# Kernel tuning notes

Hardware: AMD Instinct MI355X
Metric: run time of the kernel (lower is better)

The kernel has to match this reference:

```python
import jax, jax.numpy as jnp
import numpy as np
from jax import lax

B, S, E, DF, H, L, V, T = 32, 512, 512, 2048, 8, 2, 30000, 12
START, STOP = 10, 11
NEG = -10000.0


def setup_inputs() -> dict:
    key = jax.random.key(0)
    ks = jax.random.split(key, 12)
    g = lambda i, shape, sc=0.02: jax.random.normal(ks[i], shape, jnp.float32) * sc
    trans = jax.random.normal(ks[9], (T, T), jnp.float32)
    trans = trans.at[START, :].set(NEG).at[:, STOP].set(NEG)
    return {
        "sentence": jax.random.randint(ks[0], (B, S), 0, V),
        "seq_len": jax.random.randint(ks[1], (B,), 1, S + 1),
        "tags": jax.random.randint(ks[2], (B, S), 0, 10),
        "emb": g(3, (V, E), 1.0),
        "attn_in_w": g(4, (L, 3 * E, E)), "attn_in_b": jnp.zeros((L, 3 * E)),
        "attn_out_w": g(5, (L, E, E)), "attn_out_b": jnp.zeros((L, E)),
        "ln1_g": jnp.ones((L, E)), "ln1_b": jnp.zeros((L, E)),
        "ln2_g": jnp.ones((L, E)), "ln2_b": jnp.zeros((L, E)),
        "ff1_w": g(6, (L, DF, E)), "ff1_b": jnp.zeros((L, DF)),
        "ff2_w": g(7, (L, E, DF)), "ff2_b": jnp.zeros((L, E)),
        "tag_w": g(8, (T, E)), "tag_b": jnp.zeros((T,)),
        "transitions": trans,
    }


def _ln(x, g, b):
    m = x.mean(-1, keepdims=True)
    v = ((x - m) ** 2).mean(-1, keepdims=True)
    return (x - m) / jnp.sqrt(v + 1e-5) * g + b


def _mha(x, w_in, b_in, w_out, b_out):
    b_, s_, e_ = x.shape
    d = e_ // H
    qkv = x @ w_in.T + b_in
    q, k, v = jnp.split(qkv, 3, axis=-1)
    split = lambda t: t.reshape(b_, s_, H, d).transpose(0, 2, 1, 3)
    q, k, v = split(q), split(k), split(v)
    att = jax.nn.softmax(jnp.einsum('bhqd,bhkd->bhqk', q, k) / np.sqrt(d).astype(np.float32), axis=-1)
    o = jnp.einsum('bhqk,bhkd->bhqd', att, v).transpose(0, 2, 1, 3).reshape(b_, s_, e_)
    return o @ w_out.T + b_out


def _forward_impl(sentence, seq_len, tags, emb, attn_in_w, attn_in_b, attn_out_w,
                  attn_out_b, ln1_g, ln1_b, ln2_g, ln2_b, ff1_w, ff1_b, ff2_w,
                  ff2_b, tag_w, tag_b, transitions):
    # Transformer encoder features (dropout in eval mode -> identity)
    x = emb[sentence]  # (B,S,E)
    for l in range(L):
        x = _ln(x + _mha(x, attn_in_w[l], attn_in_b[l], attn_out_w[l], attn_out_b[l]), ln1_g[l], ln1_b[l])
        h = jax.nn.relu(x @ ff1_w[l].T + ff1_b[l]) @ ff2_w[l].T + ff2_b[l]
        x = _ln(x + h, ln2_g[l], ln2_b[l])
    feats = x @ tag_w.T + tag_b  # (B,S,T)

    # CRF forward algorithm (log-semiring scan, masked by seq_len)
    alpha0 = jnp.full((B, T), NEG, feats.dtype).at[:, START].set(0.0)

    def step(alpha, xs):
        emit_t, t = xs  # emit_t: (B,T)
        new = emit_t + jax.nn.logsumexp(alpha[:, None, :] + transitions[None, :, :], axis=-1)
        return jnp.where((t < seq_len)[:, None], new, alpha), None

    alpha, _ = lax.scan(step, alpha0, (feats.transpose(1, 0, 2), jnp.arange(S)))
    fwd_score = jax.nn.logsumexp(alpha + transitions[STOP][None, :], axis=-1)  # (B,)

    # gold score (vectorized _score_sentence)
    tags_ext = jnp.concatenate([jnp.full((B, 1), START, tags.dtype), tags], axis=1)  # (B,S+1)
    mask = jnp.arange(S)[None, :] < seq_len[:, None]  # (B,S)
    trans_sc = jnp.where(mask, transitions[tags_ext[:, 1:], tags_ext[:, :-1]], 0.0).sum(-1)
    emit_sc = jnp.where(mask, jnp.take_along_axis(feats, tags[:, :, None], axis=2)[..., 0], 0.0).sum(-1)
    last_tag = jnp.take_along_axis(tags_ext, seq_len[:, None], axis=1)[:, 0]
    gold = trans_sc + emit_sc + transitions[STOP, last_tag]

    return jnp.mean(fwd_score - gold)


def reference(sentence, seq_len, tags, emb, attn_in_w, attn_in_b, attn_out_w,
              attn_out_b, ln1_g, ln1_b, ln2_g, ln2_b, ff1_w, ff1_b, ff2_w,
              ff2_b, tag_w, tag_b, transitions):
    return _forward_impl(sentence, seq_len, tags, emb, attn_in_w, attn_in_b,
                         attn_out_w, attn_out_b, ln1_g, ln1_b, ln2_g, ln2_b,
                         ff1_w, ff1_b, ff2_w, ff2_b, tag_w, tag_b, transitions)
```

## Files before the change

kernel.cpp:

```cpp
#include <hip/hip_runtime.h>
#include <hip/hip_bf16.h>

#define BB 32
#define SSZ 512
#define EE 512
#define DFF 2048
#define HH 8
#define LL 2
#define TT 12
#define START_TAG 10
#define STOP_TAG 11
#define CB 8
#define CM (CB * SSZ)
#define NCHUNK (BB / CB)
#define NBH (CB * HH)
#define NBH_ALL (BB * HH)
#define NCHK 8

typedef __hip_bfloat16 bf16;
typedef __attribute__((ext_vector_type(8))) short short8;
typedef __attribute__((ext_vector_type(4))) float f32x4;

__device__ __forceinline__ float b2f(bf16 x) { return __bfloat162float(x); }
__device__ __forceinline__ float ldw(const void* p, size_t i, bool isbf) {
  return isbf ? __bfloat162float(((const bf16*)p)[i]) : ((const float*)p)[i];
}

__device__ __forceinline__ void gl_lds16(const bf16* g, bf16* l) {
  __builtin_amdgcn_global_load_lds(
      (const __attribute__((address_space(1))) void*)g,
      (__attribute__((address_space(3))) void*)l, 16, 0, 0);
}

__device__ __forceinline__ int swz(int row, int col) {
  return row * 128 + (col ^ (((row >> 2) & 7) * 16));
}

__global__ void k_detect(const void* trans, int* dflag) {
  if (threadIdx.x == 0) {
    const unsigned short* u = (const unsigned short*)trans;
    dflag[0] = (u[START_TAG * TT] == 0xC61C && u[START_TAG * TT + 1] == 0xC61C) ? 1 : 0;
  }
}

__global__ void k_cvt(const void* src, bf16* dst, long n, const int* dflag) {
  bool isbf = dflag[0] != 0;
  for (long i = (long)blockIdx.x * 256 + threadIdx.x; i < n; i += (long)gridDim.x * 256)
    dst[i] = __float2bfloat16(ldw(src, i, isbf));
}

__global__ void k_embed(const int* sent, const void* emb, bf16* xb, const int* dflag) {
  bool isbf = dflag[0] != 0;
  int tok = blockIdx.x;
  int v = sent[tok];
  bf16* xo = xb + (size_t)tok * EE;
  for (int i = threadIdx.x; i < EE; i += 256)
    xo[i] = __float2bfloat16(ldw(emb, (size_t)v * EE + i, isbf));
}

__global__ __launch_bounds__(256) void k_mgemm(
    const bf16* __restrict__ A, const bf16* __restrict__ W,
    const void* __restrict__ bias, size_t boff, bf16* __restrict__ Cb,
    bf16* __restrict__ vtout, int M, int N, int K, int relu, const int* dflag) {
  bool isbf = dflag[0] != 0;
  __shared__ __align__(16) bf16 Sh[2 * 128 * 64];
  bf16* As = Sh;
  bf16* Bs = Sh + 128 * 64;
  const int tid = threadIdx.x;
  const int lane = tid & 63;
  const int wave = tid >> 6;
  const int wm = wave >> 1, wn = wave & 1;
  const int m0 = blockIdx.x * 128, n0 = blockIdx.y * 128;
  const int lrow = lane & 15, lk = lane >> 4;
  const int rl = lane >> 3, sl = lane & 7;

  f32x4 acc[4][4];
#pragma unroll
  for (int i = 0; i < 4; ++i)
#pragma unroll
    for (int j = 0; j < 4; ++j) acc[i][j] = (f32x4){0.f, 0.f, 0.f, 0.f};

  for (int kt = 0; kt < K; kt += 64) {
#pragma unroll
    for (int i = 0; i < 4; ++i) {
      int r = wave * 32 + i * 8 + rl;
      int gs = sl ^ (r & 7);
      gl_lds16(A + (size_t)(m0 + r) * K + kt + gs * 8, As + wave * 2048 + i * 512);
      gl_lds16(W + (size_t)(n0 + r) * K + kt + gs * 8, Bs + wave * 2048 + i * 512);
    }
    __syncthreads();
#pragma unroll
    for (int kb = 0; kb < 64; kb += 32) {
      short8 af[4], bfr[4];
#pragma unroll
      for (int mf = 0; mf < 4; ++mf) {
        int r = wm * 64 + mf * 16 + lrow;
        int ps = ((kb >> 3) + lk) ^ (r & 7);
        af[mf] = *(const short8*)&As[r * 64 + ps * 8];
      }
#pragma unroll
      for (int nf = 0; nf < 4; ++nf) {
        int r = wn * 64 + nf * 16 + lrow;
        int ps = ((kb >> 3) + lk) ^ (r & 7);
        bfr[nf] = *(const short8*)&Bs[r * 64 + ps * 8];
      }
#pragma unroll
      for (int mf = 0; mf < 4; ++mf)
#pragma unroll
        for (int nf = 0; nf < 4; ++nf)
          acc[mf][nf] = __builtin_amdgcn_mfma_f32_16x16x32_bf16(
              af[mf], bfr[nf], acc[mf][nf], 0, 0, 0);
    }
    __syncthreads();
  }

  const bool vpath = (vtout != nullptr) && (n0 >= 1024);
  if (!vpath) {
#pragma unroll
    for (int nf = 0; nf < 4; ++nf) {
      int nl = wn * 64 + nf * 16 + lrow;
      float bia = ldw(bias, boff + n0 + nl, isbf);
#pragma unroll
      for (int mf = 0; mf < 4; ++mf) {
#pragma unroll
        for (int r = 0; r < 4; ++r) {
          int ml = wm * 64 + mf * 16 + lk * 4 + r;
          float v = acc[mf][nf][r] + bia;
          if (relu) v = fmaxf(v, 0.f);
          Sh[swz(ml, nl)] = __float2bfloat16(v);
        }
      }
    }
    __syncthreads();
#pragma unroll
    for (int p = 0; p < 8; ++p) {
      int row = p * 16 + (tid >> 4);
      int off = (tid & 15) * 8;
      *(uint4*)(Cb + (size_t)(m0 + row) * N + n0 + off) =
          *(const uint4*)&Sh[swz(row, off)];
    }
  } else {
#pragma unroll
    for (int nf = 0; nf < 4; ++nf) {
      int nl = wn * 64 + nf * 16 + lrow;
      float bia = ldw(bias, boff + n0 + nl, isbf);
#pragma unroll
      for (int mf = 0; mf < 4; ++mf) {
        int mlb = wm * 64 + mf * 16 + lk * 4;
        bf16 t4[4];
#pragma unroll
        for (int r = 0; r < 4; ++r) t4[r] = __float2bfloat16(acc[mf][nf][r] + bia);
        *(uint2*)&Sh[swz(nl, mlb)] = *(const uint2*)t4;
      }
    }
    __syncthreads();
    int h0 = (n0 - 1024) >> 6;
    int blb = (m0 >> 9) * 8;
    int pos0 = m0 & 511;
#pragma unroll
    for (int p = 0; p < 8; ++p) {
      int drow = p * 16 + (tid >> 4);
      int poff = (tid & 15) * 8;
      bf16* dst = vtout + ((size_t)(blb + h0 + (drow >> 6)) * 64 + (drow & 63)) * 512 +
                  pos0 + poff;
      *(uint4*)dst = *(const uint4*)&Sh[swz(drow, poff)];
    }
  }
}

#define LDK 68
#define LDP 72
__global__ __launch_bounds__(256) void k_flash(const bf16* __restrict__ qkv,
                                               const bf16* __restrict__ vt,
                                               bf16* __restrict__ ctx) {
  const int bh = blockIdx.x;
  const int bl = bh >> 3, h = bh & 7;
  const int m0 = blockIdx.y * 128;
  const int tid = threadIdx.x;
  const int lane = tid & 63;
  const int w = tid >> 6;
  const int lrow = lane & 15, lk = lane >> 4;

  __shared__ bf16 Ks[64 * LDK];
  __shared__ bf16 Vs[64 * LDK];
  __shared__ bf16 Ps[4][32 * LDP];

  short8 qf[2][2];
  {
    const bf16* Qb = qkv + (size_t)(bl * SSZ + m0 + w * 32) * 1536 + h * 64;
#pragma unroll
    for (int mf = 0; mf < 2; ++mf)
#pragma unroll
      for (int kb = 0; kb < 2; ++kb)
        qf[mf][kb] = *(const short8*)(Qb + (size_t)(mf * 16 + lrow) * 1536 + kb * 32 + lk * 8);
  }

  f32x4 acc_o[2][4];
  float lsum[2][4];
#pragma unroll
  for (int mf = 0; mf < 2; ++mf) {
#pragma unroll
    for (int nf = 0; nf < 4; ++nf) acc_o[mf][nf] = (f32x4){0.f, 0.f, 0.f, 0.f};
#pragma unroll
    for (int r = 0; r < 4; ++r) lsum[mf][r] = 0.f;
  }

  for (int kt = 0; kt < 8; ++kt) {
#pragma unroll
    for (int i = 0; i < 2; ++i) {
      int cc = tid + i * 256;
      int row = cc >> 3, seg = cc & 7;
      *(uint4*)&Ks[row * LDK + seg * 8] = *(const uint4*)(
          qkv + (size_t)(bl * SSZ + kt * 64 + row) * 1536 + 512 + h * 64 + seg * 8);
      *(uint4*)&Vs[row * LDK + seg * 8] = *(const uint4*)(
          vt + ((size_t)bh * 64 + row) * SSZ + kt * 64 + seg * 8);
    }
    __syncthreads();
    f32x4 s[2][4];
#pragma unroll
    for (int mf = 0; mf < 2; ++mf)
#pragma unroll
      for (int nf = 0; nf < 4; ++nf) s[mf][nf] = (f32x4){0.f, 0.f, 0.f, 0.f};
#pragma unroll
    for (int kb = 0; kb < 2; ++kb) {
      short8 bk[4];
#pragma unroll
      for (int nf = 0; nf < 4; ++nf)
        bk[nf] = *(const short8*)&Ks[(nf * 16 + lrow) * LDK + kb * 32 + lk * 8];
#pragma unroll
      for (int mf = 0; mf < 2; ++mf)
#pragma unroll
        for (int nf = 0; nf < 4; ++nf)
          s[mf][nf] = __builtin_amdgcn_mfma_f32_16x16x32_bf16(qf[mf][kb], bk[nf],
                                                              s[mf][nf], 0, 0, 0);
    }
#pragma unroll
    for (int mf = 0; mf < 2; ++mf)
#pragma unroll
      for (int r = 0; r < 4; ++r) {
        float p0 = __expf(0.125f * s[mf][0][r]);
        float p1 = __expf(0.125f * s[mf][1][r]);
        float p2 = __expf(0.125f * s[mf][2][r]);
        float p3 = __expf(0.125f * s[mf][3][r]);
        s[mf][0][r] = p0; s[mf][1][r] = p1; s[mf][2][r] = p2; s[mf][3][r] = p3;
        lsum[mf][r] += (p0 + p1) + (p2 + p3);
      }
#pragma unroll
    for (int mf = 0; mf < 2; ++mf)
#pragma unroll
      for (int nf = 0; nf < 4; ++nf)
#pragma unroll
        for (int r = 0; r < 4; ++r)
          Ps[w][(mf * 16 + lk * 4 + r) * LDP + nf * 16 + lrow] =
              __float2bfloat16(s[mf][nf][r]);
#pragma unroll
    for (int kb = 0; kb < 2; ++kb) {
      short8 ap[2], bv[4];
#pragma unroll
      for (int mf = 0; mf < 2; ++mf)
        ap[mf] = *(const short8*)&Ps[w][(mf * 16 + lrow) * LDP + kb * 32 + lk * 8];
#pragma unroll
      for (int nf = 0; nf < 4; ++nf)
        bv[nf] = *(const short8*)&Vs[(nf * 16 + lrow) * LDK + kb * 32 + lk * 8];
#pragma unroll
      for (int mf = 0; mf < 2; ++mf)
#pragma unroll
        for (int nf = 0; nf < 4; ++nf)
          acc_o[mf][nf] = __builtin_amdgcn_mfma_f32_16x16x32_bf16(ap[mf], bv[nf],
                                                                  acc_o[mf][nf], 0, 0, 0);
    }
    __syncthreads();
  }
#pragma unroll
  for (int mf = 0; mf < 2; ++mf) {
#pragma unroll
    for (int r = 0; r < 4; ++r) {
      float ls = lsum[mf][r];
      ls += __shfl_xor(ls, 1, 64);
      ls += __shfl_xor(ls, 2, 64);
      ls += __shfl_xor(ls, 4, 64);
      ls += __shfl_xor(ls, 8, 64);
      float inv = 1.f / ls;
      int q = m0 + w * 32 + mf * 16 + lk * 4 + r;
#pragma unroll
      for (int nf = 0; nf < 4; ++nf)
        ctx[((size_t)(bl * SSZ + q)) * EE + h * 64 + nf * 16 + lrow] =
            __float2bfloat16(acc_o[mf][nf][r] * inv);
    }
  }
}

__global__ void k_ln_res(bf16* xb, const bf16* hb, const void* g,
                         const void* be, size_t goff, const int* dflag) {
  bool isbf = dflag[0] != 0;
  int tok = blockIdx.x, tid = threadIdx.x;
  size_t base = (size_t)tok * EE;
  float v0 = b2f(xb[base + tid]) + b2f(hb[base + tid]);
  float v1 = b2f(xb[base + tid + 256]) + b2f(hb[base + tid + 256]);
  float s = v0 + v1, ss = v0 * v0 + v1 * v1;
#pragma unroll
  for (int off = 32; off > 0; off >>= 1) {
    s += __shfl_down(s, off, 64);
    ss += __shfl_down(ss, off, 64);
  }
  __shared__ float ps[4], pss[4];
  __shared__ float mean_s, rstd_s;
  int w = tid >> 6;
  if ((tid & 63) == 0) { ps[w] = s; pss[w] = ss; }
  __syncthreads();
  if (tid == 0) {
    float S_ = ps[0] + ps[1] + ps[2] + ps[3];
    float SS_ = pss[0] + pss[1] + pss[2] + pss[3];
    float mu = S_ / (float)EE;
    float var = SS_ / (float)EE - mu * mu;
    mean_s = mu;
    rstd_s = rsqrtf(var + 1e-5f);
  }
  __syncthreads();
  float mu = mean_s, rs = rstd_s;
  float r0 = (v0 - mu) * rs * ldw(g, goff + tid, isbf) + ldw(be, goff + tid, isbf);
  float r1 = (v1 - mu) * rs * ldw(g, goff + tid + 256, isbf) + ldw(be, goff + tid + 256, isbf);
  xb[base + tid] = __float2bfloat16(r0);
  xb[base + tid + 256] = __float2bfloat16(r1);
}

__global__ void k_feats(const bf16* xb, const bf16* tgw, const void* tgb,
                        float* feats, const int* dflag) {
  bool isbf = dflag[0] != 0;
  int m = blockIdx.x * 4 + (threadIdx.x >> 6);
  int lane = threadIdx.x & 63;
  uint4 raw = *(const uint4*)(xb + (size_t)m * EE + lane * 8);
  const bf16* rb = (const bf16*)&raw;
  float xv[8];
#pragma unroll
  for (int j = 0; j < 8; ++j) xv[j] = b2f(rb[j]);
#pragma unroll
  for (int t = 0; t < TT; ++t) {
    uint4 wraw = *(const uint4*)(tgw + t * EE + lane * 8);
    const bf16* wb = (const bf16*)&wraw;
    float s = 0.f;
#pragma unroll
    for (int j = 0; j < 8; ++j) s += xv[j] * b2f(wb[j]);
#pragma unroll
    for (int off = 32; off > 0; off >>= 1) s += __shfl_down(s, off, 64);
    if (lane == 0) feats[(size_t)m * TT + t] = s + ldw(tgb, t, isbf);
  }
}

__global__ void k_crf1(const float* feats, const int* seq_len, const void* trans_in,
                       float* cmat, const int* dflag) {
  bool isbf = dflag[0] != 0;
  int c = blockIdx.x, b = blockIdx.y;
  int tid = threadIdx.x;
  __shared__ float tr[144];
  __shared__ float abuf[2][144];
  if (tid < 144) tr[tid] = ldw(trans_in, tid, isbf);
  bool act = tid < 144;
  int i = tid / 12, j = tid % 12;
  if (act) abuf[0][tid] = (i == j) ? 0.f : -1e30f;
  __syncthreads();
  float trrow[12];
  if (act) {
#pragma unroll
    for (int k = 0; k < 12; ++k) trrow[k] = tr[i * 12 + k];
  }
  int len = seq_len[b];
  int t0 = c * 64;
  int t1 = min(len, t0 + 64);
  int cur = 0;
  for (int t = t0; t < t1; ++t) {
    float nv = 0.f;
    if (act) {
      float m = -1e30f, v[12];
#pragma unroll
      for (int k = 0; k < 12; ++k) {
        v[k] = trrow[k] + abuf[cur][k * 12 + j];
        m = fmaxf(m, v[k]);
      }
      float s = 0.f;
#pragma unroll
      for (int k = 0; k < 12; ++k) s += __expf(v[k] - m);
      nv = feats[((size_t)b * SSZ + t) * TT + i] + m + __logf(s);
    }
    if (act) abuf[cur ^ 1][tid] = nv;
    __syncthreads();
    cur ^= 1;
  }
  if (act) cmat[((size_t)b * NCHK + c) * 144 + tid] = abuf[cur][tid];
}

__global__ void k_crf2(const float* cmat, const float* feats, const int* tags,
                       const int* seq_len, const void* trans_in, float* bscore,
                       const int* dflag) {
  bool isbf = dflag[0] != 0;
  int b = blockIdx.x;
  int tid = threadIdx.x;
  __shared__ float tr[144];
  __shared__ float tbuf[2][144];
  __shared__ float alpha_sh[12];
  if (tid < 144) tr[tid] = ldw(trans_in, tid, isbf);
  bool act = tid < 144;
  int i = tid / 12, j = tid % 12;
  if (act) tbuf[0][tid] = cmat[((size_t)b * NCHK) * 144 + tid];
  __syncthreads();
  int cur = 0;
  for (int c = 1; c < NCHK; ++c) {
    float nv = 0.f;
    if (act) {
      const float* Cc = cmat + ((size_t)b * NCHK + c) * 144;
      float m = -1e30f, v[12];
#pragma unroll
      for (int k = 0; k < 12; ++k) {
        v[k] = Cc[i * 12 + k] + tbuf[cur][k * 12 + j];
        m = fmaxf(m, v[k]);
      }
      float s = 0.f;
#pragma unroll
      for (int k = 0; k < 12; ++k) s += __expf(v[k] - m);
      nv = m + __logf(s);
    }
    if (act) tbuf[cur ^ 1][tid] = nv;
    __syncthreads();
    cur ^= 1;
  }
  if (tid < 12) {
    float m = -1e30f, v[12];
#pragma unroll
    for (int k = 0; k < 12; ++k) {
      float a0 = (k == START_TAG) ? 0.f : -10000.f;
      v[k] = tbuf[cur][tid * 12 + k] + a0;
      m = fmaxf(m, v[k]);
    }
    float s = 0.f;
#pragma unroll
    for (int k = 0; k < 12; ++k) s += __expf(v[k] - m);
    alpha_sh[tid] = m + __logf(s);
  }
  __syncthreads();
  if (tid < 64) {
    int lane = tid;
    int len = seq_len[b];
    float part = 0.f;
    for (int s = lane; s < len; s += 64) {
      int ct = tags[b * SSZ + s];
      int pv = (s == 0) ? START_TAG : tags[b * SSZ + s - 1];
      part += tr[ct * 12 + pv] + feats[((size_t)b * SSZ + s) * TT + ct];
    }
#pragma unroll
    for (int off = 32; off > 0; off >>= 1) part += __shfl_down(part, off, 64);
    if (lane == 0) {
      float m = -1e30f;
#pragma unroll
      for (int k = 0; k < 12; ++k) m = fmaxf(m, alpha_sh[k] + tr[STOP_TAG * 12 + k]);
      float s = 0.f;
#pragma unroll
      for (int k = 0; k < 12; ++k) s += __expf(alpha_sh[k] + tr[STOP_TAG * 12 + k] - m);
      float fwd = m + __logf(s);
      int last = tags[b * SSZ + len - 1];
      bscore[b] = fwd - (part + tr[STOP_TAG * 12 + last]);
    }
  }
}

__global__ void k_final(const float* bscore, float* out) {
  int tid = threadIdx.x;
  float v = (tid < BB) ? bscore[tid] : 0.f;
#pragma unroll
  for (int off = 32; off > 0; off >>= 1) v += __shfl_down(v, off, 64);
  if (tid == 0) out[0] = v / (float)BB;
}

extern "C" void kernel_launch(void* const* d_in, const int* in_sizes, int n_in,
                              void* d_out, int out_size, void* d_ws, size_t ws_size,
                              hipStream_t stream) {
  const int* sentence = (const int*)d_in[0];
  const int* seq_len = (const int*)d_in[1];
  const int* tags = (const int*)d_in[2];
  const void* emb = d_in[3];
  const void* attn_in_w = d_in[4];
  const void* attn_in_b = d_in[5];
  const void* attn_out_w = d_in[6];
  const void* attn_out_b = d_in[7];
  const void* ln1_g = d_in[8];
  const void* ln1_b = d_in[9];
  const void* ln2_g = d_in[10];
  const void* ln2_b = d_in[11];
  const void* ff1_w = d_in[12];
  const void* ff1_b = d_in[13];
  const void* ff2_w = d_in[14];
  const void* ff2_b = d_in[15];
  const void* tag_w = d_in[16];
  const void* tag_b = d_in[17];
  const void* transitions = d_in[18];

  const int M = BB * SSZ;
  const size_t WEL = (size_t)LL * 3 * EE * EE + (size_t)LL * EE * EE +
                     (size_t)LL * DFF * EE + (size_t)LL * EE * DFF + (size_t)TT * EE;

  size_t o = 0;
  size_t f_feats = o; o += (size_t)M * TT;
  size_t f_bsc = o; o += 64;
  size_t f_cmat = o; o += (size_t)BB * NCHK * 144;
  size_t f_dflag = o; o += 16;
  size_t f_xb = o; o += (size_t)M * EE / 2;
  size_t f_hb = o; o += (size_t)M * EE / 2;
  size_t f_ctxb = o; o += (size_t)M * EE / 2;
  size_t f_act = o; o += (size_t)M * DFF / 2;
  size_t f_vt = o; o += (size_t)NBH_ALL * 64 * SSZ / 2;
  size_t f_w = o; o += (WEL + 1) / 2 + 8;
  size_t need_full = o * 4;
  bool full = ws_size >= need_full;

  float* ws = (float*)d_ws;
  if (full) {
    float* feats = ws + f_feats;
    float* bsc = ws + f_bsc;
    float* cmat = ws + f_cmat;
    int* dflag = (int*)(ws + f_dflag);
    bf16* xb = (bf16*)(ws + f_xb);
    bf16* hb = (bf16*)(ws + f_hb);
    bf16* ctxb = (bf16*)(ws + f_ctxb);
    bf16* act = (bf16*)(ws + f_act);
    bf16* vt = (bf16*)(ws + f_vt);
    bf16* w_aiw = (bf16*)(ws + f_w);
    bf16* w_aow = w_aiw + (size_t)LL * 3 * EE * EE;
    bf16* w_f1 = w_aow + (size_t)LL * EE * EE;
    bf16* w_f2 = w_f1 + (size_t)LL * DFF * EE;
    bf16* w_tg = w_f2 + (size_t)LL * EE * DFF;

    k_detect<<<dim3(1), dim3(64), 0, stream>>>(transitions, dflag);
    k_cvt<<<dim3(1024), dim3(256), 0, stream>>>(attn_in_w, w_aiw, (long)LL * 3 * EE * EE, dflag);
    k_cvt<<<dim3(512), dim3(256), 0, stream>>>(attn_out_w, w_aow, (long)LL * EE * EE, dflag);
    k_cvt<<<dim3(1024), dim3(256), 0, stream>>>(ff1_w, w_f1, (long)LL * DFF * EE, dflag);
    k_cvt<<<dim3(1024), dim3(256), 0, stream>>>(ff2_w, w_f2, (long)LL * EE * DFF, dflag);
    k_cvt<<<dim3(24), dim3(256), 0, stream>>>(tag_w, w_tg, (long)TT * EE, dflag);
    k_embed<<<dim3(M), dim3(256), 0, stream>>>(sentence, emb, xb, dflag);

    for (int l = 0; l < LL; ++l) {
      k_mgemm<<<dim3(M / 128, 12), dim3(256), 0, stream>>>(
          xb, w_aiw + (size_t)l * 3 * EE * EE, attn_in_b, (size_t)l * 3 * EE,
          act, vt, M, 3 * EE, EE, 0, dflag);
      k_flash<<<dim3(NBH_ALL, SSZ / 128), dim3(256), 0, stream>>>(act, vt, ctxb);
      k_mgemm<<<dim3(M / 128, 4), dim3(256), 0, stream>>>(
          ctxb, w_aow + (size_t)l * EE * EE, attn_out_b, (size_t)l * EE,
          hb, (bf16*)nullptr, M, EE, EE, 0, dflag);
      k_ln_res<<<dim3(M), dim3(256), 0, stream>>>(xb, hb, ln1_g, ln1_b,
                                                  (size_t)l * EE, dflag);
      k_mgemm<<<dim3(M / 128, 16), dim3(256), 0, stream>>>(
          xb, w_f1 + (size_t)l * DFF * EE, ff1_b, (size_t)l * DFF,
          act, (bf16*)nullptr, M, DFF, EE, 1, dflag);
      k_mgemm<<<dim3(M / 128, 4), dim3(256), 0, stream>>>(
          act, w_f2 + (size_t)l * EE * DFF, ff2_b, (size_t)l * EE,
          hb, (bf16*)nullptr, M, EE, DFF, 0, dflag);
      k_ln_res<<<dim3(M), dim3(256), 0, stream>>>(xb, hb, ln2_g, ln2_b,
                                                  (size_t)l * EE, dflag);
    }
    k_feats<<<dim3(M / 4), dim3(256), 0, stream>>>(xb, w_tg, tag_b, feats, dflag);
    k_crf1<<<dim3(NCHK, BB), dim3(192), 0, stream>>>(feats, seq_len, transitions, cmat, dflag);
    k_crf2<<<dim3(BB), dim3(192), 0, stream>>>(cmat, feats, tags, seq_len, transitions, bsc, dflag);
    k_final<<<dim3(1), dim3(64), 0, stream>>>(bsc, (float*)d_out);
  } else {
    float* feats = ws;
    float* bsc = feats + (size_t)M * TT;
    float* cmat = bsc + 64;
    int* dflag = (int*)(cmat + (size_t)BB * NCHK * 144 + 16);
    bf16* xb = (bf16*)(dflag + 16);
    bf16* hb = xb + (size_t)M * EE;
    bf16* qkvb = hb + (size_t)CM * EE;
    bf16* ctxb = qkvb + (size_t)CM * 1536;
    bf16* ffh = ctxb + (size_t)CM * EE;
    bf16* vt = ffh + (size_t)CM * DFF;
    bf16* w_aiw = vt + (size_t)NBH * 64 * SSZ;
    bf16* w_aow = w_aiw + (size_t)LL * 3 * EE * EE;
    bf16* w_f1 = w_aow + (size_t)LL * EE * EE;
    bf16* w_f2 = w_f1 + (size_t)LL * DFF * EE;
    bf16* w_tg = w_f2 + (size_t)LL * EE * DFF;

    k_detect<<<dim3(1), dim3(64), 0, stream>>>(transitions, dflag);
    k_cvt<<<dim3(1024), dim3(256), 0, stream>>>(attn_in_w, w_aiw, (long)LL * 3 * EE * EE, dflag);
    k_cvt<<<dim3(512), dim3(256), 0, stream>>>(attn_out_w, w_aow, (long)LL * EE * EE, dflag);
    k_cvt<<<dim3(1024), dim3(256), 0, stream>>>(ff1_w, w_f1, (long)LL * DFF * EE, dflag);
    k_cvt<<<dim3(1024), dim3(256), 0, stream>>>(ff2_w, w_f2, (long)LL * EE * DFF, dflag);
    k_cvt<<<dim3(24), dim3(256), 0, stream>>>(tag_w, w_tg, (long)TT * EE, dflag);
    k_embed<<<dim3(M), dim3(256), 0, stream>>>(sentence, emb, xb, dflag);

    for (int l = 0; l < LL; ++l) {
      for (int c = 0; c < NCHUNK; ++c) {
        bf16* xbc = xb + (size_t)c * CM * EE;
        k_mgemm<<<dim3(CM / 128, 12), dim3(256), 0, stream>>>(
            xbc, w_aiw + (size_t)l * 3 * EE * EE, attn_in_b, (size_t)l * 3 * EE,
            qkvb, vt, CM, 3 * EE, EE, 0, dflag);
        k_flash<<<dim3(NBH, SSZ / 128), dim3(256), 0, stream>>>(qkvb, vt, ctxb);
        k_mgemm<<<dim3(CM / 128, 4), dim3(256), 0, stream>>>(
            ctxb, w_aow + (size_t)l * EE * EE, attn_out_b, (size_t)l * EE,
            hb, (bf16*)nullptr, CM, EE, EE, 0, dflag);
        k_ln_res<<<dim3(CM), dim3(256), 0, stream>>>(xbc, hb, ln1_g, ln1_b,
                                                     (size_t)l * EE, dflag);
        k_mgemm<<<dim3(CM / 128, 16), dim3(256), 0, stream>>>(
            xbc, w_f1 + (size_t)l * DFF * EE, ff1_b, (size_t)l * DFF,
            ffh, (bf16*)nullptr, CM, DFF, EE, 1, dflag);
        k_mgemm<<<dim3(CM / 128, 4), dim3(256), 0, stream>>>(
            ffh, w_f2 + (size_t)l * EE * DFF, ff2_b, (size_t)l * EE,
            hb, (bf16*)nullptr, CM, EE, DFF, 0, dflag);
        k_ln_res<<<dim3(CM), dim3(256), 0, stream>>>(xbc, hb, ln2_g, ln2_b,
                                                     (size_t)l * EE, dflag);
      }
    }
    k_feats<<<dim3(M / 4), dim3(256), 0, stream>>>(xb, w_tg, tag_b, feats, dflag);
    k_crf1<<<dim3(NCHK, BB), dim3(192), 0, stream>>>(feats, seq_len, transitions, cmat, dflag);
    k_crf2<<<dim3(BB), dim3(192), 0, stream>>>(cmat, feats, tags, seq_len, transitions, bsc, dflag);
    k_final<<<dim3(1), dim3(64), 0, stream>>>(bsc, (float*)d_out);
  }
}
```

Before: 708.7 us.

## Skip weight conversion when inputs are bf16 and rewrite layernorm as wave-per-token

Weight conversion kernels now exit early when the detected input dtype is bf16, and the GEMM and tag-projection kernels read the original weight buffers directly in that case instead of a converted copy. The residual layernorm kernel now handles one token per 64-lane wave with 16-byte vector loads and stores and a shuffle-only reduction, dropping the shared-memory stage and the two block barriers. This removes redundant copy traffic and launch work when inputs are already bf16. It does nothing extra when inputs are fp32, where the conversion still runs.

```diff
diff --git a/kernel.cpp b/kernel.cpp
--- a/kernel.cpp
+++ b/kernel.cpp
@@ -25,6 +25,9 @@
 __device__ __forceinline__ float ldw(const void* p, size_t i, bool isbf) {
   return isbf ? __bfloat162float(((const bf16*)p)[i]) : ((const float*)p)[i];
 }
+__device__ __forceinline__ const bf16* wsel(const void* orig, const bf16* conv, bool isbf) {
+  return isbf ? (const bf16*)orig : conv;
+}
 
 __device__ __forceinline__ void gl_lds16(const bf16* g, bf16* l) {
   __builtin_amdgcn_global_load_lds(
@@ -44,9 +47,9 @@
 }
 
 __global__ void k_cvt(const void* src, bf16* dst, long n, const int* dflag) {
-  bool isbf = dflag[0] != 0;
+  if (dflag[0] != 0) return;
   for (long i = (long)blockIdx.x * 256 + threadIdx.x; i < n; i += (long)gridDim.x * 256)
-    dst[i] = __float2bfloat16(ldw(src, i, isbf));
+    dst[i] = __float2bfloat16(((const float*)src)[i]);
 }
 
 __global__ void k_embed(const int* sent, const void* emb, bf16* xb, const int* dflag) {
@@ -59,10 +62,12 @@
 }
 
 __global__ __launch_bounds__(256) void k_mgemm(
-    const bf16* __restrict__ A, const bf16* __restrict__ W,
-    const void* __restrict__ bias, size_t boff, bf16* __restrict__ Cb,
-    bf16* __restrict__ vtout, int M, int N, int K, int relu, const int* dflag) {
+    const bf16* __restrict__ A, const void* __restrict__ Worig,
+    const bf16* __restrict__ Wconv, const void* __restrict__ bias, size_t boff,
+    bf16* __restrict__ Cb, bf16* __restrict__ vtout,
+    int M, int N, int K, int relu, const int* dflag) {
   bool isbf = dflag[0] != 0;
+  const bf16* W = wsel(Worig, Wconv, isbf);
   __shared__ __align__(16) bf16 Sh[2 * 128 * 64];
   bf16* As = Sh;
   bf16* Bs = Sh + 128 * 64;
@@ -290,43 +295,46 @@
   }
 }
 
-__global__ void k_ln_res(bf16* xb, const bf16* hb, const void* g,
-                         const void* be, size_t goff, const int* dflag) {
+__global__ __launch_bounds__(256) void k_ln_res(bf16* xb, const bf16* hb,
+                                                const void* g, const void* be,
+                                                size_t goff, const int* dflag) {
   bool isbf = dflag[0] != 0;
-  int tok = blockIdx.x, tid = threadIdx.x;
-  size_t base = (size_t)tok * EE;
-  float v0 = b2f(xb[base + tid]) + b2f(hb[base + tid]);
-  float v1 = b2f(xb[base + tid + 256]) + b2f(hb[base + tid + 256]);
-  float s = v0 + v1, ss = v0 * v0 + v1 * v1;
-#pragma unroll
-  for (int off = 32; off > 0; off >>= 1) {
-    s += __shfl_down(s, off, 64);
-    ss += __shfl_down(ss, off, 64);
-  }
-  __shared__ float ps[4], pss[4];
-  __shared__ float mean_s, rstd_s;
-  int w = tid >> 6;
-  if ((tid & 63) == 0) { ps[w] = s; pss[w] = ss; }
-  __syncthreads();
-  if (tid == 0) {
-    float S_ = ps[0] + ps[1] + ps[2] + ps[3];
-    float SS_ = pss[0] + pss[1] + pss[2] + pss[3];
-    float mu = S_ / (float)EE;
-    float var = SS_ / (float)EE - mu * mu;
-    mean_s = mu;
-    rstd_s = rsqrtf(var + 1e-5f);
-  }
-  __syncthreads();
-  float mu = mean_s, rs = rstd_s;
-  float r0 = (v0 - mu) * rs * ldw(g, goff + tid, isbf) + ldw(be, goff + tid, isbf);
-  float r1 = (v1 - mu) * rs * ldw(g, goff + tid + 256, isbf) + ldw(be, goff + tid + 256, isbf);
-  xb[base + tid] = __float2bfloat16(r0);
-  xb[base + tid + 256] = __float2bfloat16(r1);
-}
-
-__global__ void k_feats(const bf16* xb, const bf16* tgw, const void* tgb,
-                        float* feats, const int* dflag) {
+  int tok = blockIdx.x * 4 + (threadIdx.x >> 6);
+  int lane = threadIdx.x & 63;
+  size_t base = (size_t)tok * EE + lane * 8;
+  uint4 xr = *(const uint4*)(xb + base);
+  uint4 hr = *(const uint4*)(hb + base);
+  const bf16* xv = (const bf16*)&xr;
+  const bf16* hv = (const bf16*)&hr;
+  float v[8];
+  float s = 0.f, ss = 0.f;
+#pragma unroll
+  for (int j = 0; j < 8; ++j) {
+    v[j] = b2f(xv[j]) + b2f(hv[j]);
+    s += v[j];
+    ss += v[j] * v[j];
+  }
+#pragma unroll
+  for (int off = 1; off < 64; off <<= 1) {
+    s += __shfl_xor(s, off, 64);
+    ss += __shfl_xor(ss, off, 64);
+  }
+  float mu = s / (float)EE;
+  float rs = rsqrtf(ss / (float)EE - mu * mu + 1e-5f);
+  bf16 outv[8];
+#pragma unroll
+  for (int j = 0; j < 8; ++j) {
+    float r = (v[j] - mu) * rs * ldw(g, goff + lane * 8 + j, isbf) +
+              ldw(be, goff + lane * 8 + j, isbf);
+    outv[j] = __float2bfloat16(r);
+  }
+  *(uint4*)(xb + base) = *(const uint4*)outv;
+}
+
+__global__ void k_feats(const bf16* xb, const void* tgorig, const bf16* tgconv,
+                        const void* tgb, float* feats, const int* dflag) {
   bool isbf = dflag[0] != 0;
+  const bf16* tgw = wsel(tgorig, tgconv, isbf);
   int m = blockIdx.x * 4 + (threadIdx.x >> 6);
   int lane = threadIdx.x & 63;
   uint4 raw = *(const uint4*)(xb + (size_t)m * EE + lane * 8);
@@ -537,25 +545,30 @@
     k_embed<<<dim3(M), dim3(256), 0, stream>>>(sentence, emb, xb, dflag);
 
     for (int l = 0; l < LL; ++l) {
+      const char* aiw_o = (const char*)attn_in_w;
+      size_t aiw_eoff = (size_t)l * 3 * EE * EE;
       k_mgemm<<<dim3(M / 128, 12), dim3(256), 0, stream>>>(
-          xb, w_aiw + (size_t)l * 3 * EE * EE, attn_in_b, (size_t)l * 3 * EE,
+          xb, aiw_o + aiw_eoff * 2, w_aiw + aiw_eoff, attn_in_b, (size_t)l * 3 * EE,
           act, vt, M, 3 * EE, EE, 0, dflag);
       k_flash<<<dim3(NBH_ALL, SSZ / 128), dim3(256), 0, stream>>>(act, vt, ctxb);
       k_mgemm<<<dim3(M / 128, 4), dim3(256), 0, stream>>>(
-          ctxb, w_aow + (size_t)l * EE * EE, attn_out_b, (size_t)l * EE,
+          ctxb, (const bf16*)attn_out_w + (size_t)l * EE * EE,
+          w_aow + (size_t)l * EE * EE, attn_out_b, (size_t)l * EE,
           hb, (bf16*)nullptr, M, EE, EE, 0, dflag);
-      k_ln_res<<<dim3(M), dim3(256), 0, stream>>>(xb, hb, ln1_g, ln1_b,
-                                                  (size_t)l * EE, dflag);
+      k_ln_res<<<dim3(M / 4), dim3(256), 0, stream>>>(xb, hb, ln1_g, ln1_b,
+                                                      (size_t)l * EE, dflag);
       k_mgemm<<<dim3(M / 128, 16), dim3(256), 0, stream>>>(
-          xb, w_f1 + (size_t)l * DFF * EE, ff1_b, (size_t)l * DFF,
+          xb, (const bf16*)ff1_w + (size_t)l * DFF * EE,
+          w_f1 + (size_t)l * DFF * EE, ff1_b, (size_t)l * DFF,
           act, (bf16*)nullptr, M, DFF, EE, 1, dflag);
       k_mgemm<<<dim3(M / 128, 4), dim3(256), 0, stream>>>(
-          act, w_f2 + (size_t)l * EE * DFF, ff2_b, (size_t)l * EE,
+          act, (const bf16*)ff2_w + (size_t)l * EE * DFF,
+          w_f2 + (size_t)l * EE * DFF, ff2_b, (size_t)l * EE,
           hb, (bf16*)nullptr, M, EE, DFF, 0, dflag);
-      k_ln_res<<<dim3(M), dim3(256), 0, stream>>>(xb, hb, ln2_g, ln2_b,
-                                                  (size_t)l * EE, dflag);
-    }
-    k_feats<<<dim3(M / 4), dim3(256), 0, stream>>>(xb, w_tg, tag_b, feats, dflag);
+      k_ln_res<<<dim3(M / 4), dim3(256), 0, stream>>>(xb, hb, ln2_g, ln2_b,
+                                                      (size_t)l * EE, dflag);
+    }
+    k_feats<<<dim3(M / 4), dim3(256), 0, stream>>>(xb, tag_w, w_tg, tag_b, feats, dflag);
     k_crf1<<<dim3(NCHK, BB), dim3(192), 0, stream>>>(feats, seq_len, transitions, cmat, dflag);
     k_crf2<<<dim3(BB), dim3(192), 0, stream>>>(cmat, feats, tags, seq_len, transitions, bsc, dflag);
     k_final<<<dim3(1), dim3(64), 0, stream>>>(bsc, (float*)d_out);
@@ -588,25 +601,29 @@
       for (int c = 0; c < NCHUNK; ++c) {
         bf16* xbc = xb + (size_t)c * CM * EE;
         k_mgemm<<<dim3(CM / 128, 12), dim3(256), 0, stream>>>(
-            xbc, w_aiw + (size_t)l * 3 * EE * EE, attn_in_b, (size_t)l * 3 * EE,
+            xbc, (const bf16*)attn_in_w + (size_t)l * 3 * EE * EE,
+            w_aiw + (size_t)l * 3 * EE * EE, attn_in_b, (size_t)l * 3 * EE,
             qkvb, vt, CM, 3 * EE, EE, 0, dflag);
         k_flash<<<dim3(NBH, SSZ / 128), dim3(256), 0, stream>>>(qkvb, vt, ctxb);
         k_mgemm<<<dim3(CM / 128, 4), dim3(256), 0, stream>>>(
-            ctxb, w_aow + (size_t)l * EE * EE, attn_out_b, (size_t)l * EE,
+            ctxb, (const bf16*)attn_out_w + (size_t)l * EE * EE,
+            w_aow + (size_t)l * EE * EE, attn_out_b, (size_t)l * EE,
             hb, (bf16*)nullptr, CM, EE, EE, 0, dflag);
-        k_ln_res<<<dim3(CM), dim3(256), 0, stream>>>(xbc, hb, ln1_g, ln1_b,
-                                                     (size_t)l * EE, dflag);
+        k_ln_res<<<dim3(CM / 4), dim3(256), 0, stream>>>(xbc, hb, ln1_g, ln1_b,
+                                                         (size_t)l * EE, dflag);
         k_mgemm<<<dim3(CM / 128, 16), dim3(256), 0, stream>>>(
-            xbc, w_f1 + (size_t)l * DFF * EE, ff1_b, (size_t)l * DFF,
+            xbc, (const bf16*)ff1_w + (size_t)l * DFF * EE,
+            w_f1 + (size_t)l * DFF * EE, ff1_b, (size_t)l * DFF,
             ffh, (bf16*)nullptr, CM, DFF, EE, 1, dflag);
         k_mgemm<<<dim3(CM / 128, 4), dim3(256), 0, stream>>>(
-            ffh, w_f2 + (size_t)l * EE * DFF, ff2_b, (size_t)l * EE,
+            ffh, (const bf16*)ff2_w + (size_t)l * EE * DFF,
+            w_f2 + (size_t)l * EE * DFF, ff2_b, (size_t)l * EE,
             hb, (bf16*)nullptr, CM, EE, DFF, 0, dflag);
-        k_ln_res<<<dim3(CM), dim3(256), 0, stream>>>(xbc, hb, ln2_g, ln2_b,
-                                                     (size_t)l * EE, dflag);
-      }
-    }
-    k_feats<<<dim3(M / 4), dim3(256), 0, stream>>>(xb, w_tg, tag_b, feats, dflag);
+        k_ln_res<<<dim3(CM / 4), dim3(256), 0, stream>>>(xbc, hb, ln2_g, ln2_b,
+                                                         (size_t)l * EE, dflag);
+      }
+    }
+    k_feats<<<dim3(M / 4), dim3(256), 0, stream>>>(xb, tag_w, w_tg, tag_b, feats, dflag);
     k_crf1<<<dim3(NCHK, BB), dim3(192), 0, stream>>>(feats, seq_len, transitions, cmat, dflag);
     k_crf2<<<dim3(BB), dim3(192), 0, stream>>>(cmat, feats, tags, seq_len, transitions, bsc, dflag);
     k_final<<<dim3(1), dim3(64), 0, stream>>>(bsc, (float*)d_out);
```

Result: slower. 786.7 us (+11.0%).
